# Kernel tuning notes

Hardware: AMD Instinct MI355X
Metric: run time of the kernel (lower is better)

## Reference

```python
import jax, jax.numpy as jnp
import numpy as np

D = 1024; L = 2; H = 16; DH = 64; INNER = H * DH; MLP = 4096; E = 8; TOPK = 2
B = 4; N = 1024
SCALE = 0.02  # init std for weights to keep activations sane through depth


def _ln(x, g, b):
    m = jnp.mean(x, -1, keepdims=True)
    v = jnp.var(x, -1, keepdims=True)
    return (x - m) / jnp.sqrt(v + 1e-5) * g + b


def setup_inputs() -> dict:
    key = jax.random.key(0)
    ks = iter(jax.random.split(key, 32))
    def w(shape, s=SCALE):
        return jax.random.normal(next(ks), shape, jnp.float32) * s
    return dict(
        x=w((B, N, D), 1.0),
        ln1_g=jnp.ones((L, D)), ln1_b=jnp.zeros((L, D)),
        Wqkv=w((L, D, 3 * INNER)), bqkv=jnp.zeros((L, 3 * INNER)),
        Wo=w((L, INNER, D)), bo=jnp.zeros((L, D)),
        Wr=w((L, D, E)), br=jnp.zeros((L, E)),
        Wa1=w((L, D, MLP)), ba1=jnp.zeros((L, MLP)),
        Wa2=w((L, MLP, D)), ba2=jnp.zeros((L, D)),
        ln2_g=jnp.ones((L, D)), ln2_b=jnp.zeros((L, D)),
        Wb0=w((L, D, D)), bb0=jnp.zeros((L, D)),
        Wb1=w((L, D, D)), bb1=jnp.zeros((L, D)),
        We_p=w((L, E - 1, D, D)), be_p=jnp.zeros((L, E - 1, D)),
        We_a=w((L, E - 1, D, D)), be_a=jnp.zeros((L, E - 1, D)),
    )


def _layer(x, p):
    (g1, b1, Wqkv, bqkv, Wo, bo, Wr, br, Wa1, ba1, Wa2, ba2,
     g2, b2, W0, b0_, W1, b1_, Pw, Pb, Aw, Ab) = p
    # PreNorm multi-head self-attention + residual
    h = _ln(x, g1, b1)
    qkv = h @ Wqkv + bqkv
    q, k, v = jnp.split(qkv, 3, -1)
    def heads(t):
        return t.reshape(B, N, H, DH).transpose(0, 2, 1, 3)  # [B,H,N,DH]
    q, k, v = heads(q), heads(k), heads(v)
    att = jax.nn.softmax(jnp.einsum('bhqd,bhkd->bhqk', q, k) * DH ** -0.5, -1)
    o = jnp.einsum('bhqk,bhkd->bhqd', att, v).transpose(0, 2, 1, 3).reshape(B, N, INNER)
    x = o @ Wo + bo + x
    # router: Linear -> KeepTopK(mask non-topk to -inf) -> Softmax (eval path)
    logits = x @ Wr + br
    thr = jax.lax.top_k(logits, TOPK)[0][..., -1:]
    weights = jax.nn.softmax(jnp.where(logits < thr, -jnp.inf, logits), -1)  # [B,N,E]
    # shared base FiLM trunk
    yt = _ln(x, g2, b2)
    ytf = jax.nn.gelu(yt @ W0 + b0_, approximate=False) * (yt @ W1 + b1_)
    # NOTE: faithful to original indexing bug ff_list[idx+2]:
    # 'expert 0' output is GELU(ytf); experts 1..E-1 are FiLM Modular_Experts.
    y = weights[..., 0:1] * jax.nn.gelu(ytf, approximate=False)
    prod = jnp.einsum('bnd,edf->bnef', ytf, Pw) + Pb   # [B,N,E-1,D]
    add = jnp.einsum('bnd,edf->bnef', ytf, Aw) + Ab
    eo = prod * ytf[:, :, None, :] + add
    y = y + jnp.einsum('bne,bnef->bnf', weights[..., 1:E], eo)
    # adaptor MLP (dropout=identity in eval) + residual
    y = jax.nn.gelu(y @ Wa1 + ba1, approximate=False) @ Wa2 + ba2
    return y + x, weights


def reference(x, ln1_g, ln1_b, Wqkv, bqkv, Wo, bo, Wr, br, Wa1, ba1, Wa2, ba2,
              ln2_g, ln2_b, Wb0, bb0, Wb1, bb1, We_p, be_p, We_a, be_a):
    ws = []
    for l in range(L):
        x, w = _layer(x, (ln1_g[l], ln1_b[l], Wqkv[l], bqkv[l], Wo[l], bo[l],
                          Wr[l], br[l], Wa1[l], ba1[l], Wa2[l], ba2[l],
                          ln2_g[l], ln2_b[l], Wb0[l], bb0[l], Wb1[l], bb1[l],
                          We_p[l], be_p[l], We_a[l], be_a[l]))
        ws.append(w)
    return x, jnp.stack(ws)
```

## Files before the change

kernel.cpp:

```cpp
#include <hip/hip_runtime.h>

typedef __bf16 bf16;
typedef __bf16 bf16x8 __attribute__((ext_vector_type(8)));
typedef float f32x4 __attribute__((ext_vector_type(4)));

#define BKSZ 32
#define BKP  40

__device__ __forceinline__ float b2f(bf16 v) { return (float)v; }
__device__ __forceinline__ bf16  f2b(float v) { return (bf16)v; }
__device__ __forceinline__ float gelu_f(float x) {
  return 0.5f * x * (1.0f + erff(x * 0.70710678118654752f));
}
__device__ __forceinline__ void split2(float v, bf16& h, bf16& l) {
  h = f2b(v); l = f2b(v - b2f(h));
}

__global__ void detect_k(const void* g1, int* ctrl) {
  if (threadIdx.x == 0 && blockIdx.x == 0) {
    unsigned u = *(const unsigned*)g1;
    ctrl[0] = (u == 0x3F800000u) ? 1 : 0;
  }
}

template<int BM, int BN, int WM, int WN, int AMODE, int BMODE, int EPI>
__global__ __launch_bounds__(256) void pgemm_k(
    const void* __restrict__ Av, const void* __restrict__ Bv,
    float* __restrict__ C,
    const void* __restrict__ biasv, const int* __restrict__ dflag,
    const int* __restrict__ elist, const int* __restrict__ ecnt,
    const int* __restrict__ eoff,
    int K, int lda, int ldb, int ldc,
    long aLo, long bLo, long cLo,
    long Bofs, long biasOfs, long biasZ, int biasGate,
    long sAo, long sAi, long sBo, long sBi, long sCo, long sCi,
    int bdiv, float alpha)
{
  __shared__ alignas(16) bf16 Ah[BM * BKP];
  __shared__ alignas(16) bf16 Al[BM * BKP];
  __shared__ alignas(16) bf16 Bh[BN * BKP];
  __shared__ alignas(16) bf16 Bl[BN * BKP];
  __shared__ int ridx[BM];

  const int tid  = threadIdx.x;
  const int lane = tid & 63;
  const int wid  = tid >> 6;
  const int z    = blockIdx.z;
  const int zo   = z / bdiv;
  const int zi   = z % bdiv;
  const bool f32b = (dflag == nullptr) || (*dflag != 0);

  long Crow0;
  if (elist) {
    int cntz = ecnt[zi];
    int padc = (cntz + BM - 1) & ~(BM - 1);
    if ((int)blockIdx.y * BM >= padc) return;
    if (tid < BM) {
      int grow = blockIdx.y * BM + tid;
      ridx[tid] = (grow < cntz) ? elist[zi * 4096 + grow] : 0;
    }
    __syncthreads();
    Crow0 = (long)eoff[zi] + (long)blockIdx.y * BM;
  } else {
    Crow0 = (long)blockIdx.y * BM;
  }

  constexpr int WCOLS = BN / WN;
  const int wm = (wid / WCOLS) * WM;
  const int wn = (wid % WCOLS) * WN;
  constexpr int TM = WM / 16;
  constexpr int TN = WN / 16;

  f32x4 acc[TM][TN];
  const f32x4 zero = {0.f, 0.f, 0.f, 0.f};
#pragma unroll
  for (int i = 0; i < TM; i++)
#pragma unroll
    for (int j = 0; j < TN; j++) acc[i][j] = zero;

  const int lm = lane & 15;
  const int q  = lane >> 4;

  const bool has_bl = (BMODE != 0) || f32b;

  for (int kt = 0; kt < K; kt += BKSZ) {
    if constexpr (AMODE == 0) {
      const float* Ap = (const float*)Av;
      const float* Ab = elist ? Ap
          : (Ap + (long)zo * sAo + (long)zi * sAi + (long)blockIdx.y * BM * lda);
      for (int idx = tid; idx < BM * (BKSZ / 4); idx += 256) {
        int m  = idx >> 3;
        int k0 = (idx & 7) * 4;
        const float* src = elist
            ? (Ap + (long)ridx[m] * lda + (long)zo * sAo + kt + k0)
            : (Ab + (long)m * lda + kt + k0);
        float4 v = *reinterpret_cast<const float4*>(src);
        alignas(8) bf16 h[4], lo[4];
        split2(v.x, h[0], lo[0]); split2(v.y, h[1], lo[1]);
        split2(v.z, h[2], lo[2]); split2(v.w, h[3], lo[3]);
        *reinterpret_cast<uint2*>(&Ah[m * BKP + k0]) = *reinterpret_cast<uint2*>(h);
        *reinterpret_cast<uint2*>(&Al[m * BKP + k0]) = *reinterpret_cast<uint2*>(lo);
      }
    } else {
      const bf16* Ap = (const bf16*)Av;
      const bf16* Ab = elist ? Ap
          : (Ap + (long)zo * sAo + (long)zi * sAi + (long)blockIdx.y * BM * lda);
      for (int idx = tid; idx < BM * (BKSZ / 8); idx += 256) {
        int m  = idx >> 2;
        int k0 = (idx & 3) * 8;
        const bf16* src = elist
            ? (Ap + (long)ridx[m] * lda + (long)zo * sAo + kt + k0)
            : (Ab + (long)m * lda + kt + k0);
        *reinterpret_cast<bf16x8*>(&Ah[m * BKP + k0]) =
            *reinterpret_cast<const bf16x8*>(src);
        *reinterpret_cast<bf16x8*>(&Al[m * BKP + k0]) =
            *reinterpret_cast<const bf16x8*>(src + aLo);
      }
    }
    if constexpr (BMODE == 3) {
      const bf16* Bb = (const bf16*)Bv + Bofs + (long)zo * sBo + (long)zi * sBi
                       + (long)blockIdx.x * BN * ldb;
      for (int idx = tid; idx < BN * (BKSZ / 8); idx += 256) {
        int n  = idx >> 2;
        int k0 = (idx & 3) * 8;
        const bf16* src = Bb + (long)n * ldb + kt + k0;
        *reinterpret_cast<bf16x8*>(&Bh[n * BKP + k0]) =
            *reinterpret_cast<const bf16x8*>(src);
        *reinterpret_cast<bf16x8*>(&Bl[n * BKP + k0]) =
            *reinterpret_cast<const bf16x8*>(src + bLo);
      }
    } else if constexpr (BMODE == 2) {
      const bf16* Bb = (const bf16*)Bv + Bofs + (long)zo * sBo + (long)zi * sBi
                       + blockIdx.x * BN;
      for (int idx = tid; idx < BN * (BKSZ / 8); idx += 256) {
        int n  = idx % BN;
        int k0 = (idx / BN) * 8;
        alignas(16) bf16 h[8], l[8];
#pragma unroll
        for (int j = 0; j < 8; j++) {
          long o = (long)(kt + k0 + j) * ldb + n;
          h[j] = Bb[o];
          l[j] = Bb[o + bLo];
        }
        *reinterpret_cast<bf16x8*>(&Bh[n * BKP + k0]) = *reinterpret_cast<bf16x8*>(h);
        *reinterpret_cast<bf16x8*>(&Bl[n * BKP + k0]) = *reinterpret_cast<bf16x8*>(l);
      }
    } else if (f32b) {
      const float* Bb = (const float*)Bv + Bofs + (long)zo * sBo + (long)zi * sBi
                        + blockIdx.x * BN;
      for (int idx = tid; idx < BN * (BKSZ / 8); idx += 256) {
        int n  = idx % BN;
        int k0 = (idx / BN) * 8;
        alignas(16) bf16 h[8], lo[8];
#pragma unroll
        for (int j = 0; j < 8; j++) {
          float v = Bb[(long)(kt + k0 + j) * ldb + n];
          split2(v, h[j], lo[j]);
        }
        *reinterpret_cast<bf16x8*>(&Bh[n * BKP + k0]) = *reinterpret_cast<bf16x8*>(h);
        *reinterpret_cast<bf16x8*>(&Bl[n * BKP + k0]) = *reinterpret_cast<bf16x8*>(lo);
      }
    } else {
      const bf16* Bb = (const bf16*)Bv + Bofs + (long)zo * sBo + (long)zi * sBi
                       + blockIdx.x * BN;
      for (int idx = tid; idx < BN * (BKSZ / 8); idx += 256) {
        int n  = idx % BN;
        int k0 = (idx / BN) * 8;
        alignas(16) bf16 h[8];
#pragma unroll
        for (int j = 0; j < 8; j++) h[j] = Bb[(long)(kt + k0 + j) * ldb + n];
        *reinterpret_cast<bf16x8*>(&Bh[n * BKP + k0]) = *reinterpret_cast<bf16x8*>(h);
      }
    }
    __syncthreads();

    bf16x8 ah[TM], al[TM], bh[TN], bl[TN];
#pragma unroll
    for (int i = 0; i < TM; i++) {
      int r = (wm + i * 16 + lm) * BKP + q * 8;
      ah[i] = *reinterpret_cast<const bf16x8*>(&Ah[r]);
      al[i] = *reinterpret_cast<const bf16x8*>(&Al[r]);
    }
#pragma unroll
    for (int j = 0; j < TN; j++) {
      int r = (wn + j * 16 + lm) * BKP + q * 8;
      bh[j] = *reinterpret_cast<const bf16x8*>(&Bh[r]);
    }
    if (has_bl) {
#pragma unroll
      for (int j = 0; j < TN; j++) {
        int r = (wn + j * 16 + lm) * BKP + q * 8;
        bl[j] = *reinterpret_cast<const bf16x8*>(&Bl[r]);
      }
#pragma unroll
      for (int i = 0; i < TM; i++)
#pragma unroll
        for (int j = 0; j < TN; j++) {
          f32x4 a = acc[i][j];
          a = __builtin_amdgcn_mfma_f32_16x16x32_bf16(al[i], bh[j], a, 0, 0, 0);
          a = __builtin_amdgcn_mfma_f32_16x16x32_bf16(ah[i], bl[j], a, 0, 0, 0);
          a = __builtin_amdgcn_mfma_f32_16x16x32_bf16(ah[i], bh[j], a, 0, 0, 0);
          acc[i][j] = a;
        }
    } else {
#pragma unroll
      for (int i = 0; i < TM; i++)
#pragma unroll
        for (int j = 0; j < TN; j++) {
          f32x4 a = acc[i][j];
          a = __builtin_amdgcn_mfma_f32_16x16x32_bf16(al[i], bh[j], a, 0, 0, 0);
          a = __builtin_amdgcn_mfma_f32_16x16x32_bf16(ah[i], bh[j], a, 0, 0, 0);
          acc[i][j] = a;
        }
    }
    __syncthreads();
  }

  const int col0 = blockIdx.x * BN + wn;
  float* Cb = C + (elist ? 0L : ((long)zo * sCo + (long)zi * sCi));
#pragma unroll
  for (int i = 0; i < TM; i++) {
#pragma unroll
    for (int j = 0; j < TN; j++) {
      int gn = col0 + j * 16 + lm;
      float bv = 0.0f;
      if (biasv && (biasGate == 0 || zo == 0)) {
        long bo = biasOfs + (long)zi * biasZ + gn;
        bv = f32b ? ((const float*)biasv)[bo] : b2f(((const bf16*)biasv)[bo]);
      }
#pragma unroll
      for (int r = 0; r < 4; r++) {
        int  lrow = wm + i * 16 + q * 4 + r;
        long cidx = (Crow0 + lrow) * (long)ldc + gn;
        float v = alpha * acc[i][j][r] + bv;
        if (EPI == 0)      Cb[cidx] = v;
        else if (EPI == 2) Cb[cidx] = gelu_f(v);
        else if (EPI == 4) atomicAdd(&Cb[cidx], v);
        else if (EPI == 8 || EPI == 9) {
          float vv = (EPI == 9) ? gelu_f(v) : v;
          bf16 hh, ll; split2(vv, hh, ll);
          bf16* Cp = (bf16*)Cb;
          Cp[cidx] = hh; Cp[cidx + cLo] = ll;
        }
      }
    }
  }
}

__global__ __launch_bounds__(256) void ln_k(const float* __restrict__ x,
                                            const void* __restrict__ g,
                                            const void* __restrict__ b,
                                            int ofs, const int* __restrict__ dflag,
                                            bf16* __restrict__ out)
{
  const bool f32in = (*dflag != 0);
  const int lane = threadIdx.x & 63;
  const int t    = blockIdx.x * 4 + (threadIdx.x >> 6);
  const float* row = x + (long)t * 1024;
  float4 v[4];
  float s = 0.f, sq = 0.f;
#pragma unroll
  for (int c = 0; c < 4; c++) {
    v[c] = reinterpret_cast<const float4*>(row)[lane + c * 64];
    s  += v[c].x + v[c].y + v[c].z + v[c].w;
    sq += v[c].x * v[c].x + v[c].y * v[c].y + v[c].z * v[c].z + v[c].w * v[c].w;
  }
#pragma unroll
  for (int o = 32; o > 0; o >>= 1) { s += __shfl_xor(s, o); sq += __shfl_xor(sq, o); }
  float m    = s * (1.0f / 1024.0f);
  float var  = sq * (1.0f / 1024.0f) - m * m;
  float rstd = 1.0f / sqrtf(var + 1e-5f);
  long rb = (long)t * 1024;
#pragma unroll
  for (int c = 0; c < 4; c++) {
    int col = (lane + c * 64) * 4;
    const float* fv = reinterpret_cast<const float*>(&v[c]);
    alignas(8) bf16 hh[4], ll[4];
#pragma unroll
    for (int e = 0; e < 4; e++) {
      float gv = f32in ? ((const float*)g)[ofs + col + e] : b2f(((const bf16*)g)[ofs + col + e]);
      float bb = f32in ? ((const float*)b)[ofs + col + e] : b2f(((const bf16*)b)[ofs + col + e]);
      split2((fv[e] - m) * rstd * gv + bb, hh[e], ll[e]);
    }
    *reinterpret_cast<uint2*>(out + rb + col) = *reinterpret_cast<uint2*>(hh);
    *reinterpret_cast<uint2*>(out + 4194304 + rb + col) = *reinterpret_cast<uint2*>(ll);
  }
}

__global__ __launch_bounds__(256) void router_k(const float* __restrict__ x,
    const void* __restrict__ Wr, const void* __restrict__ br,
    int ofsW, int ofsB, const int* __restrict__ dflag,
    float* __restrict__ wts, int* __restrict__ cnt, int* __restrict__ list)
{
  const bool f32in = (*dflag != 0);
  const int lane = threadIdx.x & 63;
  const int t    = blockIdx.x * 4 + (threadIdx.x >> 6);
  float acc[8];
#pragma unroll
  for (int e = 0; e < 8; e++) acc[e] = 0.f;
  const float* row = x + (long)t * 1024;
  for (int c = 0; c < 16; c++) {
    int d = c * 64 + lane;
    float xv = row[d];
    if (f32in) {
      const float4* p = reinterpret_cast<const float4*>((const float*)Wr + ofsW + d * 8);
      float4 w0 = p[0], w1 = p[1];
      acc[0] += xv * w0.x; acc[1] += xv * w0.y; acc[2] += xv * w0.z; acc[3] += xv * w0.w;
      acc[4] += xv * w1.x; acc[5] += xv * w1.y; acc[6] += xv * w1.z; acc[7] += xv * w1.w;
    } else {
      bf16x8 w = *reinterpret_cast<const bf16x8*>((const bf16*)Wr + ofsW + d * 8);
#pragma unroll
      for (int e = 0; e < 8; e++) acc[e] += xv * (float)w[e];
    }
  }
#pragma unroll
  for (int o = 32; o > 0; o >>= 1)
#pragma unroll
    for (int e = 0; e < 8; e++) acc[e] += __shfl_xor(acc[e], o);
#pragma unroll
  for (int e = 0; e < 8; e++)
    acc[e] += f32in ? ((const float*)br)[ofsB + e] : b2f(((const bf16*)br)[ofsB + e]);
  float m1 = -1e30f, m2 = -1e30f;
#pragma unroll
  for (int e = 0; e < 8; e++) {
    float v = acc[e];
    if (v > m1) { m2 = m1; m1 = v; }
    else if (v > m2) m2 = v;
  }
  float Z = 0.f, p[8];
#pragma unroll
  for (int e = 0; e < 8; e++) {
    p[e] = (acc[e] >= m2) ? __expf(acc[e] - m1) : 0.f;
    Z += p[e];
  }
  float inv = 1.0f / Z;
  if (lane < 8) {
    wts[t * 8 + lane] = p[lane] * inv;
    if (lane >= 1 && p[lane] > 0.f) {
      int pos = atomicAdd(&cnt[lane - 1], 1);
      list[(lane - 1) * 4096 + pos] = t;
    }
  }
}

__global__ void off_k(const int* __restrict__ cnt, int* __restrict__ off) {
  if (threadIdx.x == 0 && blockIdx.x == 0) {
    int o = 0;
    for (int e = 0; e < 7; e++) { off[e] = o; o += (cnt[e] + 127) & ~127; }
  }
}
__global__ void zcnt_k(int* __restrict__ cnt) {
  if (threadIdx.x < 7 && blockIdx.x == 0) cnt[threadIdx.x] = 0;
}
__global__ __launch_bounds__(256) void zero_k(float* __restrict__ p) {
  p[(long)blockIdx.x * 256 + threadIdx.x] = 0.f;
}
__global__ __launch_bounds__(256) void zeroeo_k(float* __restrict__ p0,
                                                float* __restrict__ p1,
                                                const int* __restrict__ cnt,
                                                const int* __restrict__ off) {
  long n = (long)(off[6] + ((cnt[6] + 127) & ~127)) * 1024;
  for (long i = (long)blockIdx.x * 256 + threadIdx.x; i < n; i += (long)gridDim.x * 256) {
    p0[i] = 0.f; p1[i] = 0.f;
  }
}

__global__ __launch_bounds__(256) void softmax_k(float* __restrict__ S)
{
  const int lane = threadIdx.x & 63;
  const long r   = (long)blockIdx.x * 4 + (threadIdx.x >> 6);
  float* row = S + r * 1024;
  float4 v[4];
#pragma unroll
  for (int c = 0; c < 4; c++) v[c] = reinterpret_cast<const float4*>(row + lane * 16)[c];
  float* f = reinterpret_cast<float*>(v);
  float mx = -1e30f;
#pragma unroll
  for (int k = 0; k < 16; k++) mx = fmaxf(mx, f[k]);
#pragma unroll
  for (int o = 32; o > 0; o >>= 1) mx = fmaxf(mx, __shfl_xor(mx, o));
  float s = 0.f;
#pragma unroll
  for (int k = 0; k < 16; k++) { f[k] = __expf(f[k] - mx); s += f[k]; }
#pragma unroll
  for (int o = 32; o > 0; o >>= 1) s += __shfl_xor(s, o);
  float inv = 1.0f / s;
  alignas(16) bf16 hh[16], ll[16];
#pragma unroll
  for (int k = 0; k < 16; k++) { f[k] *= inv; split2(f[k], hh[k], ll[k]); }
  bf16* base = reinterpret_cast<bf16*>(S) + r * 2048;
  *reinterpret_cast<bf16x8*>(base + lane * 16)     = *reinterpret_cast<bf16x8*>(&hh[0]);
  *reinterpret_cast<bf16x8*>(base + lane * 16 + 8) = *reinterpret_cast<bf16x8*>(&hh[8]);
  *reinterpret_cast<bf16x8*>(base + 1024 + lane * 16)     = *reinterpret_cast<bf16x8*>(&ll[0]);
  *reinterpret_cast<bf16x8*>(base + 1024 + lane * 16 + 8) = *reinterpret_cast<bf16x8*>(&ll[8]);
}

__global__ __launch_bounds__(256) void inx_k(const void* __restrict__ xin,
                                             const int* __restrict__ dflag,
                                             float* __restrict__ out) {
  long i = (long)blockIdx.x * 256 + threadIdx.x;
  out[i] = (*dflag != 0) ? ((const float*)xin)[i] : b2f(((const bf16*)xin)[i]);
}
__global__ __launch_bounds__(256) void ytf_k(const float* __restrict__ t0,
                                             const float* __restrict__ t1,
                                             const float* __restrict__ wl,
                                             float* __restrict__ ytf,
                                             bf16* __restrict__ ytp,
                                             float* __restrict__ y) {
  long i = (long)blockIdx.x * 256 + threadIdx.x;
  float v = gelu_f(t0[i]) * t1[i];
  ytf[i] = v;
  bf16 hh, ll; split2(v, hh, ll);
  ytp[i] = hh; ytp[i + 4194304] = ll;
  y[i] = wl[(i >> 10) * 8] * gelu_f(v);
}
__global__ __launch_bounds__(256) void scatter_k(const int* __restrict__ list,
    const int* __restrict__ cnt, const int* __restrict__ off,
    const float* __restrict__ wl, const float* __restrict__ eoP,
    const float* __restrict__ eoA, const float* __restrict__ ytf,
    float* __restrict__ yac)
{
  int e  = blockIdx.x >> 5;
  int s0 = (blockIdx.x & 31) * 128;
  int ce = cnt[e];
  if (s0 >= ce) return;
  int send = min(s0 + 128, ce);
  long base = (long)off[e] * 1024;
  for (int s = s0; s < send; s++) {
    int t = list[e * 4096 + s];
    float wv = wl[t * 8 + e + 1];
    const float* sp = eoP + base + (long)s * 1024;
    const float* sa = eoA + base + (long)s * 1024;
    const float* yt = ytf + (long)t * 1024;
    float* dst = yac + (long)t * 1024;
    for (int c = threadIdx.x; c < 1024; c += 256)
      atomicAdd(&dst[c], wv * (sp[c] * yt[c] + sa[c]));
  }
}
__global__ __launch_bounds__(256) void outw_k(const float* __restrict__ xr,
                                              const float* __restrict__ wts,
                                              const int* __restrict__ dflag,
                                              void* __restrict__ out) {
  long i = (long)blockIdx.x * 256 + threadIdx.x;
  float v = (i < 4194304) ? xr[i] : wts[i - 4194304];
  if (*dflag != 0) ((float*)out)[i] = v;
  else             ((bf16*)out)[i]  = f2b(v);
}

extern "C" void kernel_launch(void* const* d_in, const int* in_sizes, int n_in,
                              void* d_out, int out_size, void* d_ws, size_t ws_size,
                              hipStream_t stream)
{
  (void)in_sizes; (void)n_in; (void)out_size; (void)ws_size;

  char* w = (char*)d_ws;
  float* x_res = (float*)w; w += 16777216;
  float* yac   = (float*)w; w += 16777216;
  float* obuf  = yac;
  float* wts   = (float*)w; w += 262144;
  int*   ctrl  = (int*)w;   w += 1024;
  int*   list  = (int*)w;   w += 131072;
  bf16*  hbuf  = (bf16*)w;  w += 16777216;
  char* RA = w;             w += 50331648;
  char* RB = w;             w += 67108864;
  bf16*  qkvf = (bf16*)RA;
  float* t0   = (float*)RA;
  float* t1   = (float*)(RA + 16777216);
  float* eoP  = (float*)RA;
  float* Sf   = (float*)RB;
  float* ytff = (float*)RB;
  float* eoA  = (float*)(RB + 16777216);
  bf16*  a1   = (bf16*)RB;
  int* flag = ctrl;
  int* cnt  = ctrl + 8;
  int* off  = ctrl + 16;

  dim3 blk(256);
  detect_k<<<1, 64, 0, stream>>>(d_in[1], ctrl);
  inx_k<<<16384, blk, 0, stream>>>(d_in[0], flag, x_res);

  for (int l = 0; l < 2; l++) {
    ln_k<<<1024, blk, 0, stream>>>(x_res, d_in[1], d_in[2], l * 1024, flag, hbuf);
    pgemm_k<128,128,64,64,1,0,8><<<dim3(24, 32, 1), blk, 0, stream>>>(
        hbuf, d_in[3], (float*)qkvf, d_in[4], flag, nullptr, nullptr, nullptr,
        1024, 1024, 3072, 3072, 4194304, 0, 12582912,
        (long)l * 3145728, (long)l * 3072, 0, 0,
        0, 0, 0, 0, 0, 0, 1, 1.0f);
    zero_k<<<16384, blk, 0, stream>>>(obuf);
    for (int b = 0; b < 4; b++) {
      pgemm_k<128,128,64,64,1,3,0><<<dim3(8, 4, 32), blk, 0, stream>>>(
          qkvf + (long)b * 3145728, qkvf, Sf, nullptr, nullptr,
          nullptr, nullptr, nullptr,
          64, 3072, 3072, 1024, 12582912, 12582912, 0,
          (long)b * 3145728 + 1024, 0, 0, 0,
          1572864, 64, 0, 64, 524288, 1048576, 16, 0.125f);
      softmax_k<<<4096, blk, 0, stream>>>(Sf);
      pgemm_k<128,64,64,32,1,2,4><<<dim3(1, 8, 64), blk, 0, stream>>>(
          Sf, qkvf, obuf + (long)b * 1048576, nullptr, nullptr,
          nullptr, nullptr, nullptr,
          256, 2048, 3072, 1024, 1024, 12582912, 0,
          (long)b * 3145728 + 2048, 0, 0, 0,
          256, 2097152, 786432, 64, 0, 64, 16, 1.0f);
    }
    pgemm_k<128,64,64,32,0,0,4><<<dim3(16, 32, 2), blk, 0, stream>>>(
        obuf, d_in[5], x_res, d_in[6], flag, nullptr, nullptr, nullptr,
        512, 1024, 1024, 1024, 0, 0, 0,
        (long)l * 1048576, (long)l * 1024, 0, 1,
        512, 0, 524288, 0, 0, 0, 1, 1.0f);

    float* wl = wts + (long)l * 32768;
    zcnt_k<<<1, 64, 0, stream>>>(cnt);
    router_k<<<1024, blk, 0, stream>>>(x_res, d_in[7], d_in[8],
                                       l * 8192, l * 8, flag, wl, cnt, list);
    off_k<<<1, 64, 0, stream>>>(cnt, off);

    zero_k<<<32768, blk, 0, stream>>>(t0);
    ln_k<<<1024, blk, 0, stream>>>(x_res, d_in[13], d_in[14], l * 1024, flag, hbuf);
    pgemm_k<128,64,64,32,1,0,4><<<dim3(16, 32, 2), blk, 0, stream>>>(
        hbuf, d_in[15], t0, d_in[16], flag, nullptr, nullptr, nullptr,
        512, 1024, 1024, 1024, 4194304, 0, 0,
        (long)l * 1048576, (long)l * 1024, 0, 1,
        512, 0, 524288, 0, 0, 0, 1, 1.0f);
    pgemm_k<128,64,64,32,1,0,4><<<dim3(16, 32, 2), blk, 0, stream>>>(
        hbuf, d_in[17], t1, d_in[18], flag, nullptr, nullptr, nullptr,
        512, 1024, 1024, 1024, 4194304, 0, 0,
        (long)l * 1048576, (long)l * 1024, 0, 1,
        512, 0, 524288, 0, 0, 0, 1, 1.0f);
    ytf_k<<<16384, blk, 0, stream>>>(t0, t1, wl, ytff, hbuf, yac);

    zeroeo_k<<<2048, blk, 0, stream>>>(eoP, eoA, cnt, off);
    pgemm_k<128,128,64,64,1,0,4><<<dim3(8, 32, 14), blk, 0, stream>>>(
        hbuf, d_in[19], eoP, d_in[20], flag, list, cnt, off,
        512, 1024, 1024, 1024, 4194304, 0, 0,
        (long)l * 7340032, (long)l * 7168, 1024, 1,
        512, 0, 524288, 1048576, 0, 0, 7, 1.0f);
    pgemm_k<128,128,64,64,1,0,4><<<dim3(8, 32, 14), blk, 0, stream>>>(
        hbuf, d_in[21], eoA, d_in[22], flag, list, cnt, off,
        512, 1024, 1024, 1024, 4194304, 0, 0,
        (long)l * 7340032, (long)l * 7168, 1024, 1,
        512, 0, 524288, 1048576, 0, 0, 7, 1.0f);
    scatter_k<<<224, blk, 0, stream>>>(list, cnt, off, wl, eoP, eoA, ytff, yac);

    pgemm_k<128,128,64,64,0,0,9><<<dim3(32, 32, 1), blk, 0, stream>>>(
        yac, d_in[9], (float*)a1, d_in[10], flag, nullptr, nullptr, nullptr,
        1024, 1024, 4096, 4096, 0, 0, 16777216,
        (long)l * 4194304, (long)l * 4096, 0, 0,
        0, 0, 0, 0, 0, 0, 1, 1.0f);
    pgemm_k<128,64,64,32,1,0,4><<<dim3(16, 32, 4), blk, 0, stream>>>(
        a1, d_in[11], x_res, d_in[12], flag, nullptr, nullptr, nullptr,
        1024, 4096, 1024, 1024, 16777216, 0, 0,
        (long)l * 4194304, (long)l * 1024, 0, 1,
        1024, 0, 1048576, 0, 0, 0, 1, 1.0f);
  }

  outw_k<<<16640, blk, 0, stream>>>(x_res, wts, flag, d_out);
}
```

Measured before the change: 4.017 ms.

## Fuse attention into a single flash-style kernel with online softmax

```diff
diff --git a/kernel.cpp b/kernel.cpp
--- a/kernel.cpp
+++ b/kernel.cpp
@@ -117,35 +117,7 @@
             *reinterpret_cast<const bf16x8*>(src + aLo);
       }
     }
-    if constexpr (BMODE == 3) {
-      const bf16* Bb = (const bf16*)Bv + Bofs + (long)zo * sBo + (long)zi * sBi
-                       + (long)blockIdx.x * BN * ldb;
-      for (int idx = tid; idx < BN * (BKSZ / 8); idx += 256) {
-        int n  = idx >> 2;
-        int k0 = (idx & 3) * 8;
-        const bf16* src = Bb + (long)n * ldb + kt + k0;
-        *reinterpret_cast<bf16x8*>(&Bh[n * BKP + k0]) =
-            *reinterpret_cast<const bf16x8*>(src);
-        *reinterpret_cast<bf16x8*>(&Bl[n * BKP + k0]) =
-            *reinterpret_cast<const bf16x8*>(src + bLo);
-      }
-    } else if constexpr (BMODE == 2) {
-      const bf16* Bb = (const bf16*)Bv + Bofs + (long)zo * sBo + (long)zi * sBi
-                       + blockIdx.x * BN;
-      for (int idx = tid; idx < BN * (BKSZ / 8); idx += 256) {
-        int n  = idx % BN;
-        int k0 = (idx / BN) * 8;
-        alignas(16) bf16 h[8], l[8];
-#pragma unroll
-        for (int j = 0; j < 8; j++) {
-          long o = (long)(kt + k0 + j) * ldb + n;
-          h[j] = Bb[o];
-          l[j] = Bb[o + bLo];
-        }
-        *reinterpret_cast<bf16x8*>(&Bh[n * BKP + k0]) = *reinterpret_cast<bf16x8*>(h);
-        *reinterpret_cast<bf16x8*>(&Bl[n * BKP + k0]) = *reinterpret_cast<bf16x8*>(l);
-      }
-    } else if (f32b) {
+    if (f32b) {
       const float* Bb = (const float*)Bv + Bofs + (long)zo * sBo + (long)zi * sBi
                         + blockIdx.x * BN;
       for (int idx = tid; idx < BN * (BKSZ / 8); idx += 256) {
@@ -247,6 +219,176 @@
   }
 }
 
+__global__ __launch_bounds__(256) void attn_k(const bf16* __restrict__ qkv,
+                                              float* __restrict__ O)
+{
+  __shared__ alignas(16) bf16 Kh[64 * 72], Kl[64 * 72];
+  __shared__ alignas(16) bf16 Vh[64 * 72], Vl[64 * 72];
+  __shared__ alignas(16) bf16 Ph[128 * 72], Pl[128 * 72];
+
+  const int tid  = threadIdx.x;
+  const int lane = tid & 63;
+  const int w    = tid >> 6;
+  const int lm   = lane & 15;
+  const int q    = lane >> 4;
+  const int h    = blockIdx.x & 15;
+  const int b    = blockIdx.x >> 4;
+  const int qt   = blockIdx.y;
+  const long QLO = 12582912;
+
+  bf16x8 aqh[2][2], aql[2][2];
+  const long tokQ = (long)b * 1024 + qt * 128 + w * 32;
+#pragma unroll
+  for (int i = 0; i < 2; i++)
+#pragma unroll
+    for (int c = 0; c < 2; c++) {
+      long o = (tokQ + i * 16 + lm) * 3072 + h * 64 + c * 32 + q * 8;
+      aqh[i][c] = *reinterpret_cast<const bf16x8*>(qkv + o);
+      aql[i][c] = *reinterpret_cast<const bf16x8*>(qkv + QLO + o);
+    }
+
+  f32x4 acc[2][4];
+  const f32x4 zero = {0.f, 0.f, 0.f, 0.f};
+  float mrun[2][4], lrun[2][4];
+#pragma unroll
+  for (int i = 0; i < 2; i++)
+#pragma unroll
+    for (int r = 0; r < 4; r++) {
+      mrun[i][r] = -1e30f; lrun[i][r] = 0.f;
+      acc[i][r] = zero;
+    }
+
+  for (int kt = 0; kt < 16; kt++) {
+    const long tokK = (long)b * 1024 + kt * 64;
+    for (int idx = tid; idx < 512; idx += 256) {
+      int n = idx >> 3, k0 = (idx & 7) * 8;
+      long o = (tokK + n) * 3072 + 1024 + h * 64 + k0;
+      *reinterpret_cast<bf16x8*>(&Kh[n * 72 + k0]) =
+          *reinterpret_cast<const bf16x8*>(qkv + o);
+      *reinterpret_cast<bf16x8*>(&Kl[n * 72 + k0]) =
+          *reinterpret_cast<const bf16x8*>(qkv + QLO + o);
+    }
+    for (int idx = tid; idx < 512; idx += 256) {
+      int n = idx & 63, k0 = (idx >> 6) * 8;
+      alignas(16) bf16 hh[8], ll[8];
+#pragma unroll
+      for (int j = 0; j < 8; j++) {
+        long o = (tokK + k0 + j) * 3072 + 2048 + h * 64 + n;
+        hh[j] = qkv[o]; ll[j] = qkv[QLO + o];
+      }
+      *reinterpret_cast<bf16x8*>(&Vh[n * 72 + k0]) = *reinterpret_cast<bf16x8*>(hh);
+      *reinterpret_cast<bf16x8*>(&Vl[n * 72 + k0]) = *reinterpret_cast<bf16x8*>(ll);
+    }
+    __syncthreads();
+
+    f32x4 s[2][4];
+#pragma unroll
+    for (int i = 0; i < 2; i++)
+#pragma unroll
+      for (int j = 0; j < 4; j++) s[i][j] = zero;
+#pragma unroll
+    for (int j = 0; j < 4; j++) {
+      int r0 = (j * 16 + lm) * 72 + q * 8;
+      bf16x8 kh0 = *reinterpret_cast<const bf16x8*>(&Kh[r0]);
+      bf16x8 kl0 = *reinterpret_cast<const bf16x8*>(&Kl[r0]);
+      bf16x8 kh1 = *reinterpret_cast<const bf16x8*>(&Kh[r0 + 32]);
+      bf16x8 kl1 = *reinterpret_cast<const bf16x8*>(&Kl[r0 + 32]);
+#pragma unroll
+      for (int i = 0; i < 2; i++) {
+        f32x4 a = s[i][j];
+        a = __builtin_amdgcn_mfma_f32_16x16x32_bf16(aql[i][0], kh0, a, 0, 0, 0);
+        a = __builtin_amdgcn_mfma_f32_16x16x32_bf16(aqh[i][0], kl0, a, 0, 0, 0);
+        a = __builtin_amdgcn_mfma_f32_16x16x32_bf16(aqh[i][0], kh0, a, 0, 0, 0);
+        a = __builtin_amdgcn_mfma_f32_16x16x32_bf16(aql[i][1], kh1, a, 0, 0, 0);
+        a = __builtin_amdgcn_mfma_f32_16x16x32_bf16(aqh[i][1], kl1, a, 0, 0, 0);
+        a = __builtin_amdgcn_mfma_f32_16x16x32_bf16(aqh[i][1], kh1, a, 0, 0, 0);
+        s[i][j] = a;
+      }
+    }
+
+#pragma unroll
+    for (int i = 0; i < 2; i++)
+#pragma unroll
+      for (int r = 0; r < 4; r++) {
+        float mx = -1e30f;
+#pragma unroll
+        for (int j = 0; j < 4; j++) {
+          s[i][j][r] *= 0.125f;
+          mx = fmaxf(mx, s[i][j][r]);
+        }
+#pragma unroll
+        for (int o = 8; o > 0; o >>= 1) mx = fmaxf(mx, __shfl_xor(mx, o));
+        float mnew = fmaxf(mrun[i][r], mx);
+        float al   = __expf(mrun[i][r] - mnew);
+        mrun[i][r] = mnew;
+        float rs = 0.f;
+#pragma unroll
+        for (int j = 0; j < 4; j++) {
+          float p = __expf(s[i][j][r] - mnew);
+          s[i][j][r] = p; rs += p;
+        }
+#pragma unroll
+        for (int o = 8; o > 0; o >>= 1) rs += __shfl_xor(rs, o);
+        lrun[i][r] = lrun[i][r] * al + rs;
+#pragma unroll
+        for (int jn = 0; jn < 4; jn++) acc[i][jn][r] *= al;
+      }
+
+#pragma unroll
+    for (int i = 0; i < 2; i++)
+#pragma unroll
+      for (int j = 0; j < 4; j++)
+#pragma unroll
+        for (int r = 0; r < 4; r++) {
+          int row = w * 32 + i * 16 + q * 4 + r;
+          bf16 hh, ll; split2(s[i][j][r], hh, ll);
+          Ph[row * 72 + j * 16 + lm] = hh;
+          Pl[row * 72 + j * 16 + lm] = ll;
+        }
+    __syncthreads();
+
+#pragma unroll
+    for (int kc = 0; kc < 2; kc++) {
+      bf16x8 pah[2], pal[2], bvh[4], bvl[4];
+#pragma unroll
+      for (int i = 0; i < 2; i++) {
+        int r0 = (w * 32 + i * 16 + lm) * 72 + kc * 32 + q * 8;
+        pah[i] = *reinterpret_cast<const bf16x8*>(&Ph[r0]);
+        pal[i] = *reinterpret_cast<const bf16x8*>(&Pl[r0]);
+      }
+#pragma unroll
+      for (int jn = 0; jn < 4; jn++) {
+        int r0 = (jn * 16 + lm) * 72 + kc * 32 + q * 8;
+        bvh[jn] = *reinterpret_cast<const bf16x8*>(&Vh[r0]);
+        bvl[jn] = *reinterpret_cast<const bf16x8*>(&Vl[r0]);
+      }
+#pragma unroll
+      for (int i = 0; i < 2; i++)
+#pragma unroll
+        for (int jn = 0; jn < 4; jn++) {
+          f32x4 a = acc[i][jn];
+          a = __builtin_amdgcn_mfma_f32_16x16x32_bf16(pal[i], bvh[jn], a, 0, 0, 0);
+          a = __builtin_amdgcn_mfma_f32_16x16x32_bf16(pah[i], bvl[jn], a, 0, 0, 0);
+          a = __builtin_amdgcn_mfma_f32_16x16x32_bf16(pah[i], bvh[jn], a, 0, 0, 0);
+          acc[i][jn] = a;
+        }
+    }
+    __syncthreads();
+  }
+
+  const long ob = (long)b * 1048576 + (long)(qt * 128 + w * 32) * 1024 + h * 64;
+#pragma unroll
+  for (int i = 0; i < 2; i++)
+#pragma unroll
+    for (int r = 0; r < 4; r++) {
+      float inv = 1.0f / lrun[i][r];
+      long ro = ob + (long)(i * 16 + q * 4 + r) * 1024;
+#pragma unroll
+      for (int jn = 0; jn < 4; jn++)
+        O[ro + jn * 16 + lm] = acc[i][jn][r] * inv;
+    }
+}
+
 __global__ __launch_bounds__(256) void ln_k(const float* __restrict__ x,
                                             const void* __restrict__ g,
                                             const void* __restrict__ b,
@@ -363,36 +505,6 @@
   for (long i = (long)blockIdx.x * 256 + threadIdx.x; i < n; i += (long)gridDim.x * 256) {
     p0[i] = 0.f; p1[i] = 0.f;
   }
-}
-
-__global__ __launch_bounds__(256) void softmax_k(float* __restrict__ S)
-{
-  const int lane = threadIdx.x & 63;
-  const long r   = (long)blockIdx.x * 4 + (threadIdx.x >> 6);
-  float* row = S + r * 1024;
-  float4 v[4];
-#pragma unroll
-  for (int c = 0; c < 4; c++) v[c] = reinterpret_cast<const float4*>(row + lane * 16)[c];
-  float* f = reinterpret_cast<float*>(v);
-  float mx = -1e30f;
-#pragma unroll
-  for (int k = 0; k < 16; k++) mx = fmaxf(mx, f[k]);
-#pragma unroll
-  for (int o = 32; o > 0; o >>= 1) mx = fmaxf(mx, __shfl_xor(mx, o));
-  float s = 0.f;
-#pragma unroll
-  for (int k = 0; k < 16; k++) { f[k] = __expf(f[k] - mx); s += f[k]; }
-#pragma unroll
-  for (int o = 32; o > 0; o >>= 1) s += __shfl_xor(s, o);
-  float inv = 1.0f / s;
-  alignas(16) bf16 hh[16], ll[16];
-#pragma unroll
-  for (int k = 0; k < 16; k++) { f[k] *= inv; split2(f[k], hh[k], ll[k]); }
-  bf16* base = reinterpret_cast<bf16*>(S) + r * 2048;
-  *reinterpret_cast<bf16x8*>(base + lane * 16)     = *reinterpret_cast<bf16x8*>(&hh[0]);
-  *reinterpret_cast<bf16x8*>(base + lane * 16 + 8) = *reinterpret_cast<bf16x8*>(&hh[8]);
-  *reinterpret_cast<bf16x8*>(base + 1024 + lane * 16)     = *reinterpret_cast<bf16x8*>(&ll[0]);
-  *reinterpret_cast<bf16x8*>(base + 1024 + lane * 16 + 8) = *reinterpret_cast<bf16x8*>(&ll[8]);
 }
 
 __global__ __launch_bounds__(256) void inx_k(const void* __restrict__ xin,
@@ -467,7 +579,6 @@
   float* t0   = (float*)RA;
   float* t1   = (float*)(RA + 16777216);
   float* eoP  = (float*)RA;
-  float* Sf   = (float*)RB;
   float* ytff = (float*)RB;
   float* eoA  = (float*)(RB + 16777216);
   bf16*  a1   = (bf16*)RB;
@@ -486,22 +597,7 @@
         1024, 1024, 3072, 3072, 4194304, 0, 12582912,
         (long)l * 3145728, (long)l * 3072, 0, 0,
         0, 0, 0, 0, 0, 0, 1, 1.0f);
-    zero_k<<<16384, blk, 0, stream>>>(obuf);
-    for (int b = 0; b < 4; b++) {
-      pgemm_k<128,128,64,64,1,3,0><<<dim3(8, 4, 32), blk, 0, stream>>>(
-          qkvf + (long)b * 3145728, qkvf, Sf, nullptr, nullptr,
-          nullptr, nullptr, nullptr,
-          64, 3072, 3072, 1024, 12582912, 12582912, 0,
-          (long)b * 3145728 + 1024, 0, 0, 0,
-          1572864, 64, 0, 64, 524288, 1048576, 16, 0.125f);
-      softmax_k<<<4096, blk, 0, stream>>>(Sf);
-      pgemm_k<128,64,64,32,1,2,4><<<dim3(1, 8, 64), blk, 0, stream>>>(
-          Sf, qkvf, obuf + (long)b * 1048576, nullptr, nullptr,
-          nullptr, nullptr, nullptr,
-          256, 2048, 3072, 1024, 1024, 12582912, 0,
-          (long)b * 3145728 + 2048, 0, 0, 0,
-          256, 2097152, 786432, 64, 0, 64, 16, 1.0f);
-    }
+    attn_k<<<dim3(64, 8, 1), blk, 0, stream>>>(qkvf, obuf);
     pgemm_k<128,64,64,32,0,0,4><<<dim3(16, 32, 2), blk, 0, stream>>>(
         obuf, d_in[5], x_res, d_in[6], flag, nullptr, nullptr, nullptr,
         512, 1024, 1024, 1024, 0, 0, 0,
```

New measurement: 3.557 ms. 1.13x faster.
